# Kernel tuning notes

Hardware: AMD Instinct MI355X
Metric: run time of the kernel (lower is better)

Reference implementation:

```python
import jax, jax.numpy as jnp
import numpy as np

NS = 10        # number of unrolled MAP stages
N_GD = 300     # inner gradient-descent iterations
LIMS = jnp.array([3.0, 6.0, 50.0], jnp.float32)  # A_max, B_max, R1_max


def range_constraint_R1(x):
    # clip channels (A, B, R1) to [0, max] per channel
    return jnp.clip(x, 0.0, LIMS)


def physical_model(x, tau0):
    # MOLLI T1 signal model: s(tau) = A - B * exp(-tau * R1)  (signed=True)
    # x: [B,H,W,3] -> channels A, B, R1 ; tau0: [Nq]
    A = x[..., 0:1]
    Bp = x[..., 1:2]
    R1 = x[..., 2:3]
    return A - Bp * jnp.exp(-tau0 * R1)  # [B,H,W,Nq]


def dc_loss(x, b, tau0):
    s = physical_model(x, tau0)
    return 0.5 * jnp.sum(jnp.mean(jnp.square(s - b), axis=-1))


def conv2d(x, w, bias):
    y = jax.lax.conv_general_dilated(x, w, (1, 1), 'SAME',
                                     dimension_numbers=('NHWC', 'HWIO', 'NHWC'))
    return y + bias


def denoiser(x, W1, b1, Wm, bm, Wl, bl):
    # residual CNN: Nconv=7 (1 in-conv + 5 mid-convs + 1 out-conv), ReLU between
    h = jax.nn.relu(conv2d(x, W1, b1))
    for j in range(Wm.shape[0]):  # 5 structurally-distinct mid convs
        h = jax.nn.relu(conv2d(h, Wm[j], bm[j]))
    h = conv2d(h, Wl, bl)
    return x - h


def setup_inputs():
    key = jax.random.key(0)
    ks = jax.random.split(key, 8)
    B, H, W, Nq = 8, 192, 192, 11
    b = jax.random.uniform(ks[0], (B, H, W, Nq), jnp.float32)
    tau = jax.random.uniform(ks[1], (1, Nq), jnp.float32) * 3.0  # inversion times in [0,3] s
    mu = 0.01 * jnp.ones((NS,), jnp.float32)
    lm = 0.01 * jnp.ones((NS,), jnp.float32)

    def he(k, shape):
        fan_in = shape[-4] * shape[-3] * shape[-2]  # kh*kw*cin
        return jax.random.normal(k, shape, jnp.float32) * np.float32(np.sqrt(2.0 / fan_in))

    W1 = he(ks[2], (NS, 3, 3, 3, 64))
    b1 = jnp.zeros((NS, 64), jnp.float32)
    Wm = he(ks[3], (NS, 5, 3, 3, 64, 64))
    bm = jnp.zeros((NS, 5, 64), jnp.float32)
    Wl = he(ks[4], (NS, 3, 3, 64, 3))
    bl = jnp.zeros((NS, 3), jnp.float32)
    return {"b": b, "tau": tau, "mu": mu, "lm": lm,
            "W1": W1, "b1": b1, "Wm": Wm, "bm": bm, "Wl": Wl, "bl": bl}


def reference(b, tau, mu, lm, W1, b1, Wm, bm, Wl, bl):
    tau0 = tau[0]
    grad_dc = jax.grad(dc_loss)

    # init: A = max|b| over echoes, B = 2A, R1 = 1
    A = jnp.max(jnp.abs(b), axis=-1)
    x = range_constraint_R1(jnp.stack([A, 2.0 * A, jnp.ones_like(A)], axis=-1))
    xm = [x]  # test_mode=True

    @jax.checkpoint
    def gd_step(xc, _):
        gx = grad_dc(xc, b, tau0)
        gx = jnp.where(jnp.isnan(gx) | jnp.isinf(gx), 0.0, gx)
        return range_constraint_R1(xc - 2.0 * gx), None

    x, _ = jax.lax.scan(gd_step, x, None, length=N_GD)
    xm.append(x)

    for i in range(NS):
        Dx = denoiser(x, W1[i], b1[i], Wm[i], bm[i], Wl[i], bl[i])
        # Verbatim from the source: Dx is immediately overwritten with the
        # range-constrained x (source passes x, not Dx, to range_constaint_R1).
        Dx = range_constraint_R1(x)
        gx = grad_dc(x, b, tau0)
        d = gx + lm[i] * (x - Dx)
        x = range_constraint_R1(x - mu[i] * d)
        xm.append(x)

    return jnp.stack(xm)  # [NS+2, B, H, W, 3]
```

## Files before the change

kernel.cpp:

```cpp
#include <hip/hip_runtime.h>

#define NQ 11
#define NGD 300
#define NS 10


#if __has_builtin(__builtin_amdgcn_exp2f)
__device__ __forceinline__ float fexp2(float x) { return __builtin_amdgcn_exp2f(x); }
#else
__device__ __forceinline__ float fexp2(float x) {
    float r; asm("v_exp_f32 %0, %1" : "=v"(r) : "v"(x)); return r;
}
#endif

#if __has_builtin(__builtin_amdgcn_fmed3f)
__device__ __forceinline__ float clampm(float x, float lo, float hi) {
    return __builtin_amdgcn_fmed3f(x, lo, hi);
}
#else
__device__ __forceinline__ float clampm(float x, float lo, float hi) {
    return fminf(fmaxf(x, lo), hi);
}
#endif

__global__ __launch_bounds__(64) void dop_fit_kernel(
    const float* __restrict__ b,
    const float* __restrict__ tau,
    const float* __restrict__ mu,
    float* __restrict__ out,
    int P)
{
    const int p = blockIdx.x * blockDim.x + threadIdx.x;
    if (p >= P) return;

    const float LOG2E = 1.44269504088896340736f;
    float bq[NQ], tq[NQ], cq[NQ];
#pragma unroll
    for (int q = 0; q < NQ; ++q) {
        bq[q] = b[(size_t)p * NQ + q];
        tq[q] = tau[q];
        cq[q] = -tq[q] * LOG2E;
    }

    float A = 0.0f;
#pragma unroll
    for (int q = 0; q < NQ; ++q) A = fmaxf(A, fabsf(bq[q]));

    float xA = fminf(A, 3.0f);
    float xB = fminf(2.0f * A, 6.0f);
    float xR = 1.0f;

    const size_t stride = (size_t)P * 3u;
    size_t o = (size_t)p * 3u;
    out[o + 0] = xA; out[o + 1] = xB; out[o + 2] = xR;

    const float inv11 = 1.0f / 11.0f;

    auto step = [&](float a) {
        float sA = 0.0f, sE = 0.0f, sTE = 0.0f;
#pragma unroll
        for (int q = 0; q < NQ; ++q) {
            float e  = fexp2(cq[q] * xR);
            float r  = fmaf(-xB, e, xA - bq[q]);
            sA += r;
            float re = r * e;
            sE += re;
            sTE = fmaf(re, tq[q], sTE);
        }
        float mR = a * xB;
        xA = clampm(fmaf(-a, sA, xA), 0.0f, 3.0f);
        xB = clampm(fmaf( a, sE, xB), 0.0f, 6.0f);
        xR = clampm(fmaf(-mR, sTE, xR), 0.0f, 50.0f);
    };

    const float aGD = 2.0f * inv11;
    for (int it = 0; it < NGD; ++it) step(aGD);

    o += stride;
    out[o + 0] = xA; out[o + 1] = xB; out[o + 2] = xR;

    for (int i = 0; i < NS; ++i) {
        step(mu[i] * inv11);
        o += stride;
        out[o + 0] = xA; out[o + 1] = xB; out[o + 2] = xR;
    }
}

extern "C" void kernel_launch(void* const* d_in, const int* in_sizes, int n_in,
                              void* d_out, int out_size, void* d_ws, size_t ws_size,
                              hipStream_t stream) {
    const float* b   = (const float*)d_in[0];
    const float* tau = (const float*)d_in[1];
    const float* mu  = (const float*)d_in[2];
    float* out = (float*)d_out;

    const int P = in_sizes[0] / NQ;
    const int block = 64;
    const int grid = (P + block - 1) / block;
    dop_fit_kernel<<<grid, block, 0, stream>>>(b, tau, mu, out, P);
}
```

Measured before the change: 245.7 us.

## Pack per-echo math into float2 vector ops and exit GD loop early at fixed point

Rewrites the inner per-echo loop to work on float2 vectors, so packed FMA/add/mul instructions (v_pk_fma_f32 etc. on CDNA) can process two echoes at once, with the 11th echo handled as a scalar tail. The GD loop now runs two steps per iteration and breaks once every lane in the wavefront finds its state unchanged across those steps, i.e. it has reached an exact fixed point. The early exit skips work only when the iteration is stationary, so outputs should stay bit-identical. The risks are the extra compare-and-vote overhead and a summation order that differs slightly from the scalar version.

```diff
diff --git a/kernel.cpp b/kernel.cpp
--- a/kernel.cpp
+++ b/kernel.cpp
@@ -4,24 +4,23 @@
 #define NGD 300
 #define NS 10
 
+typedef float v2f __attribute__((ext_vector_type(2)));
 
+
+__device__ __forceinline__ float fexp2(float x) {
 #if __has_builtin(__builtin_amdgcn_exp2f)
-__device__ __forceinline__ float fexp2(float x) { return __builtin_amdgcn_exp2f(x); }
+    return __builtin_amdgcn_exp2f(x);
 #else
-__device__ __forceinline__ float fexp2(float x) {
     float r; asm("v_exp_f32 %0, %1" : "=v"(r) : "v"(x)); return r;
+#endif
 }
+__device__ __forceinline__ float clampm(float x, float lo, float hi) {
+#if __has_builtin(__builtin_amdgcn_fmed3f)
+    return __builtin_amdgcn_fmed3f(x, lo, hi);
+#else
+    return fminf(fmaxf(x, lo), hi);
 #endif
-
-#if __has_builtin(__builtin_amdgcn_fmed3f)
-__device__ __forceinline__ float clampm(float x, float lo, float hi) {
-    return __builtin_amdgcn_fmed3f(x, lo, hi);
 }
-#else
-__device__ __forceinline__ float clampm(float x, float lo, float hi) {
-    return fminf(fmaxf(x, lo), hi);
-}
-#endif
 
 __global__ __launch_bounds__(64) void dop_fit_kernel(
     const float* __restrict__ b,
@@ -34,13 +33,22 @@
     if (p >= P) return;
 
     const float LOG2E = 1.44269504088896340736f;
-    float bq[NQ], tq[NQ], cq[NQ];
+
+    float bq[NQ];
 #pragma unroll
-    for (int q = 0; q < NQ; ++q) {
-        bq[q] = b[(size_t)p * NQ + q];
-        tq[q] = tau[q];
-        cq[q] = -tq[q] * LOG2E;
+    for (int q = 0; q < NQ; ++q) bq[q] = b[(size_t)p * NQ + q];
+
+    v2f tq2[5], ct2[5], nb2[5];
+#pragma unroll
+    for (int j = 0; j < 5; ++j) {
+        float t0 = tau[2 * j], t1 = tau[2 * j + 1];
+        tq2[j] = (v2f){t0, t1};
+        ct2[j] = (v2f){-t0 * LOG2E, -t1 * LOG2E};
+        nb2[j] = (v2f){-bq[2 * j], -bq[2 * j + 1]};
     }
+    const float t10 = tau[10];
+    const float ct10 = -t10 * LOG2E;
+    const float nb10 = -bq[10];
 
     float A = 0.0f;
 #pragma unroll
@@ -57,24 +65,39 @@
     const float inv11 = 1.0f / 11.0f;
 
     auto step = [&](float a) {
-        float sA = 0.0f, sE = 0.0f, sTE = 0.0f;
+        v2f sA2 = (v2f){0.f, 0.f}, sE2 = (v2f){0.f, 0.f}, sT2 = (v2f){0.f, 0.f};
+        const v2f xA2  = (v2f){xA, xA};
+        const v2f nxB2 = (v2f){-xB, -xB};
 #pragma unroll
-        for (int q = 0; q < NQ; ++q) {
-            float e  = fexp2(cq[q] * xR);
-            float r  = fmaf(-xB, e, xA - bq[q]);
-            sA += r;
-            float re = r * e;
-            sE += re;
-            sTE = fmaf(re, tq[q], sTE);
+        for (int j = 0; j < 5; ++j) {
+            v2f m2 = ct2[j] * xR;
+            v2f e2; e2.x = fexp2(m2.x); e2.y = fexp2(m2.y);
+            v2f r2 = __builtin_elementwise_fma(nxB2, e2, xA2) + nb2[j];
+            sA2 += r2;
+            v2f re2 = r2 * e2;
+            sE2 += re2;
+            sT2 = __builtin_elementwise_fma(re2, tq2[j], sT2);
         }
+        float e  = fexp2(ct10 * xR);
+        float r  = fmaf(-xB, e, xA) + nb10;
+        float re = r * e;
+        float sA = (sA2.x + sA2.y) + r;
+        float sE = (sE2.x + sE2.y) + re;
+        float sT = (sT2.x + sT2.y) + re * t10;
         float mR = a * xB;
-        xA = clampm(fmaf(-a, sA, xA), 0.0f, 3.0f);
-        xB = clampm(fmaf( a, sE, xB), 0.0f, 6.0f);
-        xR = clampm(fmaf(-mR, sTE, xR), 0.0f, 50.0f);
+        xA = clampm(fmaf(-a,  sA, xA), 0.0f, 3.0f);
+        xB = clampm(fmaf( a,  sE, xB), 0.0f, 6.0f);
+        xR = clampm(fmaf(-mR, sT, xR), 0.0f, 50.0f);
     };
 
     const float aGD = 2.0f * inv11;
-    for (int it = 0; it < NGD; ++it) step(aGD);
+    for (int n = 0; n < NGD; n += 2) {
+        const float pA = xA, pB = xB, pR = xR;
+        step(aGD);
+        step(aGD);
+        if (__builtin_expect(__all((xA == pA) & (xB == pB) & (xR == pR)), 0))
+            break;
+    }
 
     o += stride;
     out[o + 0] = xA; out[o + 1] = xB; out[o + 2] = xR;
```

Measured after the change: 220.3 us. 1.12x faster.
